# Kernel optimization log

Measured on AMD Instinct MI355X. Metric: run time of the kernel, lower is better.

Reference implementation:

```python
import jax, jax.numpy as jnp
import numpy as np

B, L, D = 2, 2048, 1024
DH = 64
NH = D // DH
EPS = 1e-5
NEG = -1e30


def rms_norm(x, w):
    # x: (..., dh); norm in fp32 like the torch module, then scale by weight
    xf = x.astype(jnp.float32)
    y = xf * jax.lax.rsqrt(jnp.mean(xf * xf, axis=-1, keepdims=True) + EPS)
    return y.astype(x.dtype) * w.astype(x.dtype)


def sdpa(q, k, v, m):
    # q:(b,h,lq,dh) k,v:(b,h,lk,dh) m:(lq,lk) bool
    scale = 1.0 / jnp.sqrt(jnp.asarray(DH, q.dtype))
    s = jnp.einsum('bhqd,bhkd->bhqk', q, k) * scale
    s = jnp.where(m[None, None], s, NEG)
    p = jax.nn.softmax(s, axis=-1)
    return jnp.einsum('bhqk,bhkd->bhqd', p, v)


def setup_inputs() -> dict:
    key = jax.random.key(0)
    k1, k2, k3 = jax.random.split(key, 3)
    x = jax.random.normal(k1, (B, L, D), dtype=jnp.float32)
    mask = jnp.tril(jnp.ones((L, L), dtype=bool))  # causal: no fully-masked rows
    w_qkv = jax.random.normal(k2, (3 * D, D), dtype=jnp.float32) * (1.0 / np.sqrt(D))
    w_fc = jax.random.normal(k3, (D, D), dtype=jnp.float32) * (1.0 / np.sqrt(D))
    q_norm_w = jnp.ones((DH,), dtype=jnp.float32)
    k_norm_w = jnp.ones((DH,), dtype=jnp.float32)
    return {"x": x, "mask": mask, "w_qkv": w_qkv, "w_fc": w_fc,
            "q_norm_w": q_norm_w, "k_norm_w": k_norm_w,
            "subset_attention_size": 1024}


def reference(x, mask, w_qkv, w_fc, q_norm_w, k_norm_w, subset_attention_size):
    b, l, d = x.shape
    qkv = jnp.einsum('bld,ed->ble', x, w_qkv)  # (b,l,3d)
    q, k, v = jnp.split(qkv, 3, axis=-1)

    def heads(t):
        return t.reshape(b, l, NH, DH).transpose(0, 2, 1, 3)  # (b,nh,l,dh)

    q, k, v = heads(q), heads(k), heads(v)
    q = rms_norm(q, q_norm_w)
    k = rms_norm(k, k_norm_w)

    S = subset_attention_size
    if S is not None and S < l:
        o1 = sdpa(q[:, :, :S], k[:, :, :S], v[:, :, :S], mask[:S, :S])
        o2 = sdpa(q[:, :, S:], k, v, mask[S:, :])
        o = jnp.concatenate([o1, o2], axis=2)
    else:
        o = sdpa(q, k, v, mask)
    o = o.transpose(0, 2, 1, 3).reshape(b, l, d)  # (b,l,d)
    return jnp.einsum('bld,ed->ble', o, w_fc)
```

## Files before the change

### kernel.cpp

```cpp
#include <hip/hip_runtime.h>

typedef __bf16 bf16x8 __attribute__((ext_vector_type(8)));
typedef __bf16 bf16x4 __attribute__((ext_vector_type(4)));
typedef float f32x4 __attribute__((ext_vector_type(4)));
typedef unsigned short u16;
typedef unsigned int u32;
typedef unsigned short u16x4 __attribute__((ext_vector_type(4)));
typedef unsigned short u16x8 __attribute__((ext_vector_type(8)));

#define AS1 __attribute__((address_space(1)))
#define AS3 __attribute__((address_space(3)))

__device__ __forceinline__ u16 f2bf(float f) {
  unsigned u = __builtin_bit_cast(unsigned, f);
  u += 0x7fffu + ((u >> 16) & 1u);
  return (u16)(u >> 16);
}
__device__ __forceinline__ float bf2f(u16 h) {
  unsigned u = ((unsigned)h) << 16;
  return __builtin_bit_cast(float, u);
}

__global__ __launch_bounds__(256) void cvt_all(const float* __restrict__ x,
                                               const float* __restrict__ wq,
                                               const float* __restrict__ wf,
                                               u16* __restrict__ xb, u16* __restrict__ wqb,
                                               u16* __restrict__ wfb) {
  long i = ((long)blockIdx.x * 256 + threadIdx.x) * 4;
  const float* src;
  u16* dst;
  long off;
  if (i < 4194304L) {
    src = x; dst = xb; off = i;
  } else if (i < 7340032L) {
    src = wq; dst = wqb; off = i - 4194304L;
  } else {
    src = wf; dst = wfb; off = i - 7340032L;
  }
  float4 v = *reinterpret_cast<const float4*>(src + off);
  u16x4 o;
  o.x = f2bf(v.x); o.y = f2bf(v.y); o.z = f2bf(v.z); o.w = f2bf(v.w);
  *reinterpret_cast<u16x4*>(dst + off) = o;
}

__global__ __launch_bounds__(256, 2) void gemm_qkv(const u16* __restrict__ A,
                                                   const u16* __restrict__ W,
                                                   u16* __restrict__ C, int N, int K) {
  __shared__ __align__(16) u16 As[128 * 32];
  __shared__ __align__(16) u16 Bs[128 * 32];
  const int tid = threadIdx.x;
  const int lane = tid & 63;
  const int wid = tid >> 6;
  const int wm = wid >> 1, wn = wid & 1;
  const int l16 = lane & 15, g4 = lane >> 4;
  const long bm = blockIdx.x, bn = blockIdx.y;

  const int srow = tid >> 2;
  const int scol = (tid & 3) * 8;
  const u16* aA0 = A + (bm * 128 + srow) * (long)K + scol;
  const u16* aA1 = aA0 + 64 * (long)K;
  const u16* aW0 = W + (bn * 128 + srow) * (long)K + scol;
  const u16* aW1 = aW0 + 64 * (long)K;

  f32x4 acc[4][4] = {};

  for (int kt = 0; kt < K; kt += 32) {
    __builtin_amdgcn_global_load_lds((AS1 void*)(aA0 + kt), (AS3 void*)(&As[tid * 8]), 16, 0, 0);
    __builtin_amdgcn_global_load_lds((AS1 void*)(aA1 + kt), (AS3 void*)(&As[2048 + tid * 8]), 16, 0, 0);
    __builtin_amdgcn_global_load_lds((AS1 void*)(aW0 + kt), (AS3 void*)(&Bs[tid * 8]), 16, 0, 0);
    __builtin_amdgcn_global_load_lds((AS1 void*)(aW1 + kt), (AS3 void*)(&Bs[2048 + tid * 8]), 16, 0, 0);
    __syncthreads();
    bf16x8 af[4], bfr[4];
#pragma unroll
    for (int m = 0; m < 4; ++m)
      af[m] = *reinterpret_cast<const bf16x8*>(&As[(wm * 64 + m * 16 + l16) * 32 + g4 * 8]);
#pragma unroll
    for (int n = 0; n < 4; ++n)
      bfr[n] = *reinterpret_cast<const bf16x8*>(&Bs[(wn * 64 + n * 16 + l16) * 32 + g4 * 8]);
#pragma unroll
    for (int m = 0; m < 4; ++m)
#pragma unroll
      for (int n = 0; n < 4; ++n)
        acc[m][n] = __builtin_amdgcn_mfma_f32_16x16x32_bf16(af[m], bfr[n], acc[m][n], 0, 0, 0);
    __syncthreads();
  }

#pragma unroll
  for (int m = 0; m < 4; ++m)
#pragma unroll
    for (int n = 0; n < 4; ++n)
#pragma unroll
      for (int j = 0; j < 4; ++j) {
        long row = bm * 128 + wm * 64 + m * 16 + g4 * 4 + j;
        long col = bn * 128 + wn * 64 + n * 16 + l16;
        C[row * N + col] = f2bf(acc[m][n][j]);
      }
}

__global__ __launch_bounds__(256, 2) void gemm_fc(const u16* __restrict__ A,
                                                  const u16* __restrict__ W,
                                                  float* __restrict__ C, int N, int K) {
  __shared__ __align__(16) u16 As[128 * 32];
  __shared__ __align__(16) u16 Bs[64 * 32];
  const int tid = threadIdx.x;
  const int lane = tid & 63;
  const int wid = tid >> 6;
  const int wm = wid >> 1, wn = wid & 1;
  const int l16 = lane & 15, g4 = lane >> 4;
  const long bm = blockIdx.x, bn = blockIdx.y;

  const int srow = tid >> 2;
  const int scol = (tid & 3) * 8;
  const u16* aA0 = A + (bm * 128 + srow) * (long)K + scol;
  const u16* aA1 = aA0 + 64 * (long)K;
  const u16* aW0 = W + (bn * 64 + srow) * (long)K + scol;

  f32x4 acc[4][2] = {};

  for (int kt = 0; kt < K; kt += 32) {
    __builtin_amdgcn_global_load_lds((AS1 void*)(aA0 + kt), (AS3 void*)(&As[tid * 8]), 16, 0, 0);
    __builtin_amdgcn_global_load_lds((AS1 void*)(aA1 + kt), (AS3 void*)(&As[2048 + tid * 8]), 16, 0, 0);
    __builtin_amdgcn_global_load_lds((AS1 void*)(aW0 + kt), (AS3 void*)(&Bs[tid * 8]), 16, 0, 0);
    __syncthreads();
    bf16x8 af[4], bfr[2];
#pragma unroll
    for (int m = 0; m < 4; ++m)
      af[m] = *reinterpret_cast<const bf16x8*>(&As[(wm * 64 + m * 16 + l16) * 32 + g4 * 8]);
#pragma unroll
    for (int n = 0; n < 2; ++n)
      bfr[n] = *reinterpret_cast<const bf16x8*>(&Bs[(wn * 32 + n * 16 + l16) * 32 + g4 * 8]);
#pragma unroll
    for (int m = 0; m < 4; ++m)
#pragma unroll
      for (int n = 0; n < 2; ++n)
        acc[m][n] = __builtin_amdgcn_mfma_f32_16x16x32_bf16(af[m], bfr[n], acc[m][n], 0, 0, 0);
    __syncthreads();
  }

#pragma unroll
  for (int m = 0; m < 4; ++m)
#pragma unroll
    for (int n = 0; n < 2; ++n)
#pragma unroll
      for (int j = 0; j < 4; ++j) {
        long row = bm * 128 + wm * 64 + m * 16 + g4 * 4 + j;
        long col = bn * 64 + wn * 32 + n * 16 + l16;
        C[row * N + col] = acc[m][n][j];
      }
}

__global__ __launch_bounds__(256) void rmsnorm_qk(u16* __restrict__ qkv,
                                                  const float* __restrict__ qw,
                                                  const float* __restrict__ kw) {
  const int tid = threadIdx.x;
  const int l16 = tid & 15;
  const long row = (long)blockIdx.x * 16 + (tid >> 4);
  const int isK = row >= 65536;
  const long r = isK ? row - 65536 : row;
  const long bl = r >> 4;
  const int h = (int)(r & 15);
  u16* p = qkv + bl * 3072 + (isK ? 1024 : 0) + h * 64 + l16 * 4;
  u16x4 v = *reinterpret_cast<const u16x4*>(p);
  float f0 = bf2f(v.x), f1 = bf2f(v.y), f2 = bf2f(v.z), f3 = bf2f(v.w);
  float ss = f0 * f0 + f1 * f1 + f2 * f2 + f3 * f3;
  ss += __shfl_xor(ss, 1);
  ss += __shfl_xor(ss, 2);
  ss += __shfl_xor(ss, 4);
  ss += __shfl_xor(ss, 8);
  const float inv = rsqrtf(ss * (1.0f / 64.0f) + 1e-5f);
  const float* w = isK ? kw : qw;
  u16x4 o;
  o.x = f2bf(f0 * inv * w[l16 * 4 + 0]);
  o.y = f2bf(f1 * inv * w[l16 * 4 + 1]);
  o.z = f2bf(f2 * inv * w[l16 * 4 + 2]);
  o.w = f2bf(f3 * inv * w[l16 * 4 + 3]);
  *reinterpret_cast<u16x4*>(p) = o;
}

__global__ __launch_bounds__(256, 2) void attn_causal(const u16* __restrict__ qkv,
                                                      u16* __restrict__ o) {
  __shared__ __align__(16) u16 Klds[2][4096];
  __shared__ __align__(16) u16 Vt[2][4096];
  __shared__ __align__(16) u16 Plds[4][1024];

  const int tid = threadIdx.x, lane = tid & 63, wid = tid >> 6;
  const int l16 = lane & 15, g4 = lane >> 4;
  const int h8 = (l16 & 7) << 4;
  const int qlo = blockIdx.x, qhi = 31 - qlo;
  const int bh = blockIdx.y;
  const long base = (long)(bh >> 4) * 2048 * 3072 + (bh & 15) * 64;
  const u16* qb = qkv + base;
  const u16* kb = qkv + base + 1024;
  const u16* vb = qkv + base + 2048;

  const u16* qpA = qb + ((long)qlo * 64 + wid * 16 + l16) * 3072;
  const u16* qpB = qb + ((long)qhi * 64 + wid * 16 + l16) * 3072;
  const bf16x8 qA0 = *reinterpret_cast<const bf16x8*>(qpA + g4 * 8);
  const bf16x8 qA1 = *reinterpret_cast<const bf16x8*>(qpA + 32 + g4 * 8);
  const bf16x8 qB0 = *reinterpret_cast<const bf16x8*>(qpB + g4 * 8);
  const bf16x8 qB1 = *reinterpret_cast<const bf16x8*>(qpB + 32 + g4 * 8);

  f32x4 accA[4] = {}, accB[4] = {};
  f32x4 laccA = {}, laccB = {};
  const float cl = 0.125f * 1.4426950408889634f;
  const float mc = -8.0f * cl;

  const int krow = tid >> 3;
  const int scolE = (((tid & 7) * 16) ^ ((krow & 7) << 4)) >> 1;
  const int vkey = (lane & 31) * 2;
  const int vd = wid * 8 + (lane >> 5) * 32;

  u16x8 vv0, vv1;

  auto stage_issue = [&](int buf, int kt) {
    __builtin_amdgcn_global_load_lds((AS1 void*)(kb + (long)(kt * 64 + krow) * 3072 + scolE),
                                     (AS3 void*)(&Klds[buf][tid * 8]), 16, 0, 0);
    __builtin_amdgcn_global_load_lds((AS1 void*)(kb + (long)(kt * 64 + krow + 32) * 3072 + scolE),
                                     (AS3 void*)(&Klds[buf][2048 + tid * 8]), 16, 0, 0);
    const u16* gv = vb + (long)(kt * 64 + vkey) * 3072 + vd;
    vv0 = *reinterpret_cast<const u16x8*>(gv);
    vv1 = *reinterpret_cast<const u16x8*>(gv + 3072);
  };
  auto vt_write = [&](int buf) {
#pragma unroll
    for (int j = 0; j < 8; ++j) {
      const int r = vd + j;
      const int boff = (vkey * 2) ^ ((r & 7) << 4);
      *reinterpret_cast<u32*>(&Vt[buf][r * 64 + (boff >> 1)]) =
          (u32)vv0[j] | ((u32)vv1[j] << 16);
    }
  };

  auto tile_step = [&](f32x4* acc, f32x4& lacc, const bf16x8& q0, const bf16x8& q1, bool diag,
                       bf16x8 (&kf)[4][2], int cur) {
    f32x4 s[4];
    __builtin_amdgcn_s_setprio(1);
#pragma unroll
    for (int kn = 0; kn < 4; ++kn) {
      f32x4 z = {0.f, 0.f, 0.f, 0.f};
      z = __builtin_amdgcn_mfma_f32_16x16x32_bf16(kf[kn][0], q0, z, 0, 0, 0);
      z = __builtin_amdgcn_mfma_f32_16x16x32_bf16(kf[kn][1], q1, z, 0, 0, 0);
      s[kn] = z;
    }
    __builtin_amdgcn_s_setprio(0);
    if (diag) {
      const int qrel = wid * 16 + l16;
#pragma unroll
      for (int kn = 0; kn < 4; ++kn)
#pragma unroll
        for (int j = 0; j < 4; ++j)
          if (kn * 16 + g4 * 4 + j > qrel) s[kn][j] = -3e38f;
    }
#pragma unroll
    for (int kn = 0; kn < 4; ++kn) {
#pragma unroll
      for (int j = 0; j < 4; ++j) s[kn][j] = exp2f(fmaf(s[kn][j], cl, mc));
      lacc += s[kn];
    }
    u16* pl = &Plds[wid][0];
#pragma unroll
    for (int kn = 0; kn < 4; ++kn) {
      bf16x4 w;
      w[0] = (__bf16)s[kn][0];
      w[1] = (__bf16)s[kn][1];
      w[2] = (__bf16)s[kn][2];
      w[3] = (__bf16)s[kn][3];
      const int boff = (kn * 32 + g4 * 8) ^ h8;
      *reinterpret_cast<bf16x4*>(&pl[l16 * 64 + (boff >> 1)]) = w;
    }
    const bf16x8 pa0 = *reinterpret_cast<const bf16x8*>(&pl[l16 * 64 + (((0 * 64 + g4 * 16) ^ h8) >> 1)]);
    const bf16x8 pa1 = *reinterpret_cast<const bf16x8*>(&pl[l16 * 64 + (((1 * 64 + g4 * 16) ^ h8) >> 1)]);
    __builtin_amdgcn_s_setprio(1);
#pragma unroll
    for (int n = 0; n < 4; ++n) {
      const int rr = n * 16 + l16;
      const bf16x8 b0 =
          *reinterpret_cast<const bf16x8*>(&Vt[cur][rr * 64 + (((0 * 64 + g4 * 16) ^ h8) >> 1)]);
      const bf16x8 b1 =
          *reinterpret_cast<const bf16x8*>(&Vt[cur][rr * 64 + (((1 * 64 + g4 * 16) ^ h8) >> 1)]);
      acc[n] = __builtin_amdgcn_mfma_f32_16x16x32_bf16(pa0, b0, acc[n], 0, 0, 0);
      acc[n] = __builtin_amdgcn_mfma_f32_16x16x32_bf16(pa1, b1, acc[n], 0, 0, 0);
    }
    __builtin_amdgcn_s_setprio(0);
  };

  stage_issue(0, 0);
  vt_write(0);
  __syncthreads();

  const int nt = qhi + 1;
  for (int kt = 0; kt < nt; ++kt) {
    const int cur = kt & 1, nxt = cur ^ 1;
    const bool pre = (kt + 1 < nt);
    if (pre) stage_issue(nxt, kt + 1);

    bf16x8 kf[4][2];
#pragma unroll
    for (int kn = 0; kn < 4; ++kn) {
      const int row = kn * 16 + l16;
      kf[kn][0] = *reinterpret_cast<const bf16x8*>(&Klds[cur][row * 64 + (((g4 * 16) ^ h8) >> 1)]);
      kf[kn][1] =
          *reinterpret_cast<const bf16x8*>(&Klds[cur][row * 64 + (((64 + g4 * 16) ^ h8) >> 1)]);
    }

    if (kt <= qlo) tile_step(accA, laccA, qA0, qA1, kt == qlo, kf, cur);
    tile_step(accB, laccB, qB0, qB1, kt == qhi, kf, cur);

    if (pre) vt_write(nxt);
    __syncthreads();
  }

  const long obase = (long)(bh >> 4) * 2048 * 1024 + (bh & 15) * 64;
  auto epi = [&](f32x4* acc, f32x4 lacc, int qt) {
    float l = lacc[0] + lacc[1] + lacc[2] + lacc[3];
    l += __shfl_xor(l, 16);
    l += __shfl_xor(l, 32);
    float lR[4];
#pragma unroll
    for (int j = 0; j < 4; ++j) lR[j] = __shfl(l, g4 * 4 + j, 16);
    u16* op = o + obase + (long)(qt * 64 + wid * 16 + g4 * 4) * 1024;
#pragma unroll
    for (int n = 0; n < 4; ++n)
#pragma unroll
      for (int j = 0; j < 4; ++j)
        op[j * 1024 + n * 16 + l16] = f2bf(acc[n][j] / lR[j]);
  };
  epi(accA, laccA, qlo);
  epi(accB, laccB, qhi);
}

extern "C" void kernel_launch(void* const* d_in, const int* in_sizes, int n_in,
                              void* d_out, int out_size, void* d_ws, size_t ws_size,
                              hipStream_t stream) {
  const float* x = (const float*)d_in[0];
  const float* w_qkv = (const float*)d_in[2];
  const float* w_fc = (const float*)d_in[3];
  const float* qw = (const float*)d_in[4];
  const float* kw = (const float*)d_in[5];
  float* out = (float*)d_out;

  char* ws = (char*)d_ws;
  u16* xb    = (u16*)(ws);
  u16* wqkvb = (u16*)(ws + (8L << 20));
  u16* wfcb  = (u16*)(ws + (14L << 20));
  u16* qkv   = (u16*)(ws + (16L << 20));
  u16* ob    = (u16*)(ws + (40L << 20));

  cvt_all<<<8192, 256, 0, stream>>>(x, w_qkv, w_fc, xb, wqkvb, wfcb);

  gemm_qkv<<<dim3(32, 24), 256, 0, stream>>>(xb, wqkvb, qkv, 3072, 1024);
  rmsnorm_qk<<<8192, 256, 0, stream>>>(qkv, qw, kw);
  attn_causal<<<dim3(16, 32), 256, 0, stream>>>(qkv, ob);
  gemm_fc<<<dim3(32, 16), 256, 0, stream>>>(ob, wfcb, out, 1024, 1024);
}
```

Baseline: 117.4 us.

## Fuse QK RMSNorm into QKV GEMM epilogue and split attention keys across waves

The RMSNorm on Q and K now runs inside the QKV GEMM epilogue on the fp32 accumulators, which removes a separate kernel launch and a bf16 read-modify-write pass over Q and K. The causal attention kernel moves from 64-row to 32-row query tiles. Each block's four waves split as 2 row groups by 2 key halves, and the two key-half partial accumulators and row sums are combined through LDS at the end. This gives 1024 blocks with a higher occupancy bound of 4, in exchange for an extra LDS reduction and more K/V tile loads per query row. Normalizing in fp32 before the bf16 rounding also changes numerics slightly.

```diff
diff --git a/kernel.cpp b/kernel.cpp
--- a/kernel.cpp
+++ b/kernel.cpp
@@ -15,10 +15,6 @@
   unsigned u = __builtin_bit_cast(unsigned, f);
   u += 0x7fffu + ((u >> 16) & 1u);
   return (u16)(u >> 16);
-}
-__device__ __forceinline__ float bf2f(u16 h) {
-  unsigned u = ((unsigned)h) << 16;
-  return __builtin_bit_cast(float, u);
 }
 
 __global__ __launch_bounds__(256) void cvt_all(const float* __restrict__ x,
@@ -45,7 +41,10 @@
 
 __global__ __launch_bounds__(256, 2) void gemm_qkv(const u16* __restrict__ A,
                                                    const u16* __restrict__ W,
-                                                   u16* __restrict__ C, int N, int K) {
+                                                   u16* __restrict__ C,
+                                                   const float* __restrict__ qw,
+                                                   const float* __restrict__ kw) {
+  constexpr int N = 3072, K = 1024;
   __shared__ __align__(16) u16 As[128 * 32];
   __shared__ __align__(16) u16 Bs[128 * 32];
   const int tid = threadIdx.x;
@@ -85,6 +84,29 @@
     __syncthreads();
   }
 
+  if (bn < 16) {
+    const float* w = (bn < 8) ? qw : kw;
+    float wv[4];
+#pragma unroll
+    for (int n = 0; n < 4; ++n) wv[n] = w[n * 16 + l16];
+#pragma unroll
+    for (int m = 0; m < 4; ++m) {
+#pragma unroll
+      for (int j = 0; j < 4; ++j) {
+        float ss = 0.f;
+#pragma unroll
+        for (int n = 0; n < 4; ++n) ss = fmaf(acc[m][n][j], acc[m][n][j], ss);
+        ss += __shfl_xor(ss, 1);
+        ss += __shfl_xor(ss, 2);
+        ss += __shfl_xor(ss, 4);
+        ss += __shfl_xor(ss, 8);
+        const float inv = rsqrtf(ss * (1.0f / 64.0f) + 1e-5f);
+#pragma unroll
+        for (int n = 0; n < 4; ++n) acc[m][n][j] *= inv * wv[n];
+      }
+    }
+  }
+
 #pragma unroll
   for (int m = 0; m < 4; ++m)
 #pragma unroll
@@ -99,7 +121,8 @@
 
 __global__ __launch_bounds__(256, 2) void gemm_fc(const u16* __restrict__ A,
                                                   const u16* __restrict__ W,
-                                                  float* __restrict__ C, int N, int K) {
+                                                  float* __restrict__ C) {
+  constexpr int N = 1024, K = 1024;
   __shared__ __align__(16) u16 As[128 * 32];
   __shared__ __align__(16) u16 Bs[64 * 32];
   const int tid = threadIdx.x;
@@ -149,52 +172,29 @@
       }
 }
 
-__global__ __launch_bounds__(256) void rmsnorm_qk(u16* __restrict__ qkv,
-                                                  const float* __restrict__ qw,
-                                                  const float* __restrict__ kw) {
-  const int tid = threadIdx.x;
-  const int l16 = tid & 15;
-  const long row = (long)blockIdx.x * 16 + (tid >> 4);
-  const int isK = row >= 65536;
-  const long r = isK ? row - 65536 : row;
-  const long bl = r >> 4;
-  const int h = (int)(r & 15);
-  u16* p = qkv + bl * 3072 + (isK ? 1024 : 0) + h * 64 + l16 * 4;
-  u16x4 v = *reinterpret_cast<const u16x4*>(p);
-  float f0 = bf2f(v.x), f1 = bf2f(v.y), f2 = bf2f(v.z), f3 = bf2f(v.w);
-  float ss = f0 * f0 + f1 * f1 + f2 * f2 + f3 * f3;
-  ss += __shfl_xor(ss, 1);
-  ss += __shfl_xor(ss, 2);
-  ss += __shfl_xor(ss, 4);
-  ss += __shfl_xor(ss, 8);
-  const float inv = rsqrtf(ss * (1.0f / 64.0f) + 1e-5f);
-  const float* w = isK ? kw : qw;
-  u16x4 o;
-  o.x = f2bf(f0 * inv * w[l16 * 4 + 0]);
-  o.y = f2bf(f1 * inv * w[l16 * 4 + 1]);
-  o.z = f2bf(f2 * inv * w[l16 * 4 + 2]);
-  o.w = f2bf(f3 * inv * w[l16 * 4 + 3]);
-  *reinterpret_cast<u16x4*>(p) = o;
-}
-
-__global__ __launch_bounds__(256, 2) void attn_causal(const u16* __restrict__ qkv,
+__global__ __launch_bounds__(256, 4) void attn_causal(const u16* __restrict__ qkv,
                                                       u16* __restrict__ o) {
   __shared__ __align__(16) u16 Klds[2][4096];
   __shared__ __align__(16) u16 Vt[2][4096];
-  __shared__ __align__(16) u16 Plds[4][1024];
+  __shared__ __align__(16) u16 Plds[4][640];
 
   const int tid = threadIdx.x, lane = tid & 63, wid = tid >> 6;
   const int l16 = lane & 15, g4 = lane >> 4;
-  const int h8 = (l16 & 7) << 4;
-  const int qlo = blockIdx.x, qhi = 31 - qlo;
-  const int bh = blockIdx.y;
+  const int rh = wid & 1, kh = wid >> 1;
+
+  const int f = blockIdx.x;
+  const int kk = f >> 3;
+  const int bh = (f & 7) * 4 + (kk >> 5);
+  const int i = kk & 31;
+  const int iA = i, iB = 63 - i;
+
   const long base = (long)(bh >> 4) * 2048 * 3072 + (bh & 15) * 64;
   const u16* qb = qkv + base;
   const u16* kb = qkv + base + 1024;
   const u16* vb = qkv + base + 2048;
 
-  const u16* qpA = qb + ((long)qlo * 64 + wid * 16 + l16) * 3072;
-  const u16* qpB = qb + ((long)qhi * 64 + wid * 16 + l16) * 3072;
+  const u16* qpA = qb + ((long)iA * 32 + rh * 16 + l16) * 3072;
+  const u16* qpB = qb + ((long)iB * 32 + rh * 16 + l16) * 3072;
   const bf16x8 qA0 = *reinterpret_cast<const bf16x8*>(qpA + g4 * 8);
   const bf16x8 qA1 = *reinterpret_cast<const bf16x8*>(qpA + 32 + g4 * 8);
   const bf16x8 qB0 = *reinterpret_cast<const bf16x8*>(qpB + g4 * 8);
@@ -209,7 +209,6 @@
   const int scolE = (((tid & 7) * 16) ^ ((krow & 7) << 4)) >> 1;
   const int vkey = (lane & 31) * 2;
   const int vd = wid * 8 + (lane >> 5) * 32;
-
   u16x8 vv0, vv1;
 
   auto stage_issue = [&](int buf, int kt) {
@@ -231,55 +230,52 @@
     }
   };
 
-  auto tile_step = [&](f32x4* acc, f32x4& lacc, const bf16x8& q0, const bf16x8& q1, bool diag,
-                       bf16x8 (&kf)[4][2], int cur) {
-    f32x4 s[4];
+  auto step = [&](int qt, f32x4* acc, f32x4& lacc, const bf16x8& q0, const bf16x8& q1,
+                  bf16x8 (&kf)[2][2], int cur, int kt) {
+    const int dd = qt - 2 * kt - kh;
+    if (dd < 0) return;
+    f32x4 s[2];
     __builtin_amdgcn_s_setprio(1);
 #pragma unroll
-    for (int kn = 0; kn < 4; ++kn) {
+    for (int kn = 0; kn < 2; ++kn) {
       f32x4 z = {0.f, 0.f, 0.f, 0.f};
       z = __builtin_amdgcn_mfma_f32_16x16x32_bf16(kf[kn][0], q0, z, 0, 0, 0);
       z = __builtin_amdgcn_mfma_f32_16x16x32_bf16(kf[kn][1], q1, z, 0, 0, 0);
       s[kn] = z;
     }
     __builtin_amdgcn_s_setprio(0);
-    if (diag) {
-      const int qrel = wid * 16 + l16;
-#pragma unroll
-      for (int kn = 0; kn < 4; ++kn)
+    if (dd == 0) {
+      const int qr = rh * 16 + l16;
+#pragma unroll
+      for (int kn = 0; kn < 2; ++kn)
 #pragma unroll
         for (int j = 0; j < 4; ++j)
-          if (kn * 16 + g4 * 4 + j > qrel) s[kn][j] = -3e38f;
-    }
-#pragma unroll
-    for (int kn = 0; kn < 4; ++kn) {
+          if (kn * 16 + g4 * 4 + j > qr) s[kn][j] = -3e38f;
+    }
+#pragma unroll
+    for (int kn = 0; kn < 2; ++kn) {
 #pragma unroll
       for (int j = 0; j < 4; ++j) s[kn][j] = exp2f(fmaf(s[kn][j], cl, mc));
       lacc += s[kn];
     }
     u16* pl = &Plds[wid][0];
 #pragma unroll
-    for (int kn = 0; kn < 4; ++kn) {
-      bf16x4 w;
-      w[0] = (__bf16)s[kn][0];
-      w[1] = (__bf16)s[kn][1];
-      w[2] = (__bf16)s[kn][2];
-      w[3] = (__bf16)s[kn][3];
-      const int boff = (kn * 32 + g4 * 8) ^ h8;
-      *reinterpret_cast<bf16x4*>(&pl[l16 * 64 + (boff >> 1)]) = w;
-    }
-    const bf16x8 pa0 = *reinterpret_cast<const bf16x8*>(&pl[l16 * 64 + (((0 * 64 + g4 * 16) ^ h8) >> 1)]);
-    const bf16x8 pa1 = *reinterpret_cast<const bf16x8*>(&pl[l16 * 64 + (((1 * 64 + g4 * 16) ^ h8) >> 1)]);
+    for (int kn = 0; kn < 2; ++kn) {
+      bf16x4 w4;
+      w4[0] = (__bf16)s[kn][0];
+      w4[1] = (__bf16)s[kn][1];
+      w4[2] = (__bf16)s[kn][2];
+      w4[3] = (__bf16)s[kn][3];
+      *reinterpret_cast<bf16x4*>(&pl[l16 * 40 + kn * 16 + g4 * 4]) = w4;
+    }
+    const bf16x8 pa = *reinterpret_cast<const bf16x8*>(&pl[l16 * 40 + g4 * 8]);
     __builtin_amdgcn_s_setprio(1);
 #pragma unroll
     for (int n = 0; n < 4; ++n) {
       const int rr = n * 16 + l16;
-      const bf16x8 b0 =
-          *reinterpret_cast<const bf16x8*>(&Vt[cur][rr * 64 + (((0 * 64 + g4 * 16) ^ h8) >> 1)]);
-      const bf16x8 b1 =
-          *reinterpret_cast<const bf16x8*>(&Vt[cur][rr * 64 + (((1 * 64 + g4 * 16) ^ h8) >> 1)]);
-      acc[n] = __builtin_amdgcn_mfma_f32_16x16x32_bf16(pa0, b0, acc[n], 0, 0, 0);
-      acc[n] = __builtin_amdgcn_mfma_f32_16x16x32_bf16(pa1, b1, acc[n], 0, 0, 0);
+      const bf16x8 b = *reinterpret_cast<const bf16x8*>(
+          &Vt[cur][rr * 64 + (((kh * 64 + g4 * 16) ^ ((rr & 7) << 4)) >> 1)]);
+      acc[n] = __builtin_amdgcn_mfma_f32_16x16x32_bf16(pa, b, acc[n], 0, 0, 0);
     }
     __builtin_amdgcn_s_setprio(0);
   };
@@ -288,45 +284,73 @@
   vt_write(0);
   __syncthreads();
 
-  const int nt = qhi + 1;
-  for (int kt = 0; kt < nt; ++kt) {
+  const int ktmax = (iB >> 1) + 1;
+  for (int kt = 0; kt < ktmax; ++kt) {
     const int cur = kt & 1, nxt = cur ^ 1;
-    const bool pre = (kt + 1 < nt);
+    const bool pre = (kt + 1 < ktmax);
     if (pre) stage_issue(nxt, kt + 1);
 
-    bf16x8 kf[4][2];
-#pragma unroll
-    for (int kn = 0; kn < 4; ++kn) {
-      const int row = kn * 16 + l16;
-      kf[kn][0] = *reinterpret_cast<const bf16x8*>(&Klds[cur][row * 64 + (((g4 * 16) ^ h8) >> 1)]);
-      kf[kn][1] =
-          *reinterpret_cast<const bf16x8*>(&Klds[cur][row * 64 + (((64 + g4 * 16) ^ h8) >> 1)]);
-    }
-
-    if (kt <= qlo) tile_step(accA, laccA, qA0, qA1, kt == qlo, kf, cur);
-    tile_step(accB, laccB, qB0, qB1, kt == qhi, kf, cur);
+    bf16x8 kf[2][2];
+#pragma unroll
+    for (int kn = 0; kn < 2; ++kn) {
+      const int row = kh * 32 + kn * 16 + l16;
+#pragma unroll
+      for (int ck = 0; ck < 2; ++ck)
+        kf[kn][ck] = *reinterpret_cast<const bf16x8*>(
+            &Klds[cur][row * 64 + (((ck * 64 + g4 * 16) ^ ((l16 & 7) << 4)) >> 1)]);
+    }
+
+    step(iA, accA, laccA, qA0, qA1, kf, cur, kt);
+    step(iB, accB, laccB, qB0, qB1, kf, cur, kt);
 
     if (pre) vt_write(nxt);
     __syncthreads();
   }
 
-  const long obase = (long)(bh >> 4) * 2048 * 1024 + (bh & 15) * 64;
-  auto epi = [&](f32x4* acc, f32x4 lacc, int qt) {
-    float l = lacc[0] + lacc[1] + lacc[2] + lacc[3];
+  auto lred = [&](const f32x4& v) {
+    float l = v[0] + v[1] + v[2] + v[3];
     l += __shfl_xor(l, 16);
     l += __shfl_xor(l, 32);
-    float lR[4];
-#pragma unroll
-    for (int j = 0; j < 4; ++j) lR[j] = __shfl(l, g4 * 4 + j, 16);
-    u16* op = o + obase + (long)(qt * 64 + wid * 16 + g4 * 4) * 1024;
-#pragma unroll
-    for (int n = 0; n < 4; ++n)
-#pragma unroll
-      for (int j = 0; j < 4; ++j)
-        op[j * 1024 + n * 16 + l16] = f2bf(acc[n][j] / lR[j]);
+    return l;
   };
-  epi(accA, laccA, qlo);
-  epi(accB, laccB, qhi);
+  float lA = lred(laccA), lB = lred(laccB);
+
+  float* cbf = reinterpret_cast<float*>(&Klds[0][0]);
+  float* lvf = reinterpret_cast<float*>(&Vt[0][0]);
+  if (kh == 1) {
+#pragma unroll
+    for (int n = 0; n < 4; ++n) {
+      *reinterpret_cast<f32x4*>(&cbf[(rh * 8 + n) * 256 + lane * 4]) = accA[n];
+      *reinterpret_cast<f32x4*>(&cbf[(rh * 8 + 4 + n) * 256 + lane * 4]) = accB[n];
+    }
+    lvf[(rh * 2 + 0) * 64 + lane] = lA;
+    lvf[(rh * 2 + 1) * 64 + lane] = lB;
+  }
+  __syncthreads();
+  if (kh == 0) {
+#pragma unroll
+    for (int n = 0; n < 4; ++n) {
+      accA[n] += *reinterpret_cast<const f32x4*>(&cbf[(rh * 8 + n) * 256 + lane * 4]);
+      accB[n] += *reinterpret_cast<const f32x4*>(&cbf[(rh * 8 + 4 + n) * 256 + lane * 4]);
+    }
+    lA += lvf[(rh * 2 + 0) * 64 + lane];
+    lB += lvf[(rh * 2 + 1) * 64 + lane];
+
+    const long obase = (long)(bh >> 4) * 2048 * 1024 + (bh & 15) * 64;
+    auto epi = [&](f32x4* acc, float l, int qt) {
+      float lR[4];
+#pragma unroll
+      for (int j = 0; j < 4; ++j) lR[j] = __shfl(l, g4 * 4 + j, 16);
+      u16* op = o + obase + ((long)qt * 32 + rh * 16 + g4 * 4) * 1024;
+#pragma unroll
+      for (int n = 0; n < 4; ++n)
+#pragma unroll
+        for (int j = 0; j < 4; ++j)
+          op[j * 1024 + n * 16 + l16] = f2bf(acc[n][j] / lR[j]);
+    };
+    epi(accA, lA, iA);
+    epi(accB, lB, iB);
+  }
 }
 
 extern "C" void kernel_launch(void* const* d_in, const int* in_sizes, int n_in,
@@ -347,9 +371,7 @@
   u16* ob    = (u16*)(ws + (40L << 20));
 
   cvt_all<<<8192, 256, 0, stream>>>(x, w_qkv, w_fc, xb, wqkvb, wfcb);
-
-  gemm_qkv<<<dim3(32, 24), 256, 0, stream>>>(xb, wqkvb, qkv, 3072, 1024);
-  rmsnorm_qk<<<8192, 256, 0, stream>>>(qkv, qw, kw);
-  attn_causal<<<dim3(16, 32), 256, 0, stream>>>(qkv, ob);
-  gemm_fc<<<dim3(32, 16), 256, 0, stream>>>(ob, wfcb, out, 1024, 1024);
-}
+  gemm_qkv<<<dim3(32, 24), 256, 0, stream>>>(xb, wqkvb, qkv, qw, kw);
+  attn_causal<<<1024, 256, 0, stream>>>(qkv, ob);
+  gemm_fc<<<dim3(32, 16), 256, 0, stream>>>(ob, wfcb, out);
+}
```

New measurement: 115.7 us. Within noise of the previous version (-1.4%).
